# Kernel tuning notes

Hardware: AMD Instinct MI355X
Metric: run time of the kernel (lower is better)

Reference implementation:

```python
import jax, jax.numpy as jnp
import numpy as np

GAMMA = 1.0
ALPHA = 0.5
EPS = 1e-8


def setup_inputs() -> dict:
    key = jax.random.key(0)
    k1, k2 = jax.random.split(key)
    x = jax.random.normal(k1, (2048, 32), dtype=jnp.float32)
    y = jax.random.normal(k2, (2048, 32), dtype=jnp.float32)
    return {"x": x, "y": y}


def _normalize(a):
    # torch: mean/std over batch dim, std is unbiased (ddof=1)
    mu = jnp.mean(a, axis=0, keepdims=True)
    sd = jnp.std(a, axis=0, ddof=1, keepdims=True)
    return (a - mu) / (sd + EPS)


def reference(x, y):
    # Classical RBF kernel on normalized inputs
    xn = _normalize(x)
    yn = _normalize(y)
    d = xn[:, None, :] - yn[None, :, :]            # [N, M, D]
    classical = jnp.exp(-GAMMA * jnp.sum(d * d, axis=-1))  # [N, M]

    # Quantum kernel, analytic closed form:
    # RY(t)|0> = [cos(t/2), sin(t/2)]; product state overlap ->
    # |<psi_x|psi_y>|^2 = prod_i cos^2((x_i - y_i)/2)
    qd = (x[:, None, :] - y[None, :, :]) * 0.5     # [N, M, D]
    quantum = jnp.prod(jnp.square(jnp.cos(qd)), axis=-1)    # [N, M]

    return (1.0 - ALPHA) * classical + ALPHA * quantum
```

## Files before the change

### kernel.cpp

```cpp
#include <hip/hip_runtime.h>
#include <math.h>

#define NROWS 2048
#define DDIM 32

typedef __attribute__((ext_vector_type(8))) short short8;
typedef __attribute__((ext_vector_type(4))) float f32x4;
typedef __attribute__((ext_vector_type(2))) float f32x2;

__device__ __forceinline__ unsigned packbf(float a, float b) {
  return (__float_as_uint(a) >> 16) | (__float_as_uint(b) & 0xffff0000u);
}

__global__ __launch_bounds__(512, 2) void HybridKernel_fused(
    const float* __restrict__ x, const float* __restrict__ y,
    float* __restrict__ out) {
  __shared__ f32x4 sCSx[16 * 128];
  __shared__ f32x4 sYP[2048];
  __shared__ uint4 sXB[2][2][128 * 5];
  __shared__ f32x4 sRed[2][64][8];
  __shared__ f32x4 sRedQ[2][64][8];
  __shared__ float sNrm[2][128];
  __shared__ float sMu[2][32];
  __shared__ float sInv[2][32];

  const int t = threadIdx.x;
  const int i0 = blockIdx.y * 128;
  const int j0 = blockIdx.x * 128;

  float4 gx[2], gy[2];
#pragma unroll
  for (int rep = 0; rep < 2; ++rep) {
    const int u = t + 512 * rep;
    const int row = u >> 3;
    const int q = u & 7;
    gx[rep] = *reinterpret_cast<const float4*>(&x[(i0 + row) * DDIM + q * 4]);
    gy[rep] = *reinterpret_cast<const float4*>(&y[(j0 + row) * DDIM + q * 4]);
  }

#pragma unroll
  for (int rep = 0; rep < 2; ++rep) {
    const int u = t + 512 * rep;
    const int row = u >> 3;
    const int q = u & 7;
    {
      const float4 g = gx[rep];
      const float gv[4] = {g.x, g.y, g.z, g.w};
      float hc[4], hs[4];
#pragma unroll
      for (int k = 0; k < 4; ++k) {
        float sn, cs;
        __sincosf(gv[k], &sn, &cs);
        hc[k] = 0.5f * cs;
        hs[k] = 0.5f * sn;
      }
      const int dp0 = 2 * q, dp1 = 2 * q + 1;
      sCSx[dp0 * 128 + (row ^ (dp0 & 7))] = f32x4{hc[0], hs[0], hc[1], hs[1]};
      sCSx[dp1 * 128 + (row ^ (dp1 & 7))] = f32x4{hc[2], hs[2], hc[3], hs[3]};
    }
    {
      const float4 g = gy[rep];
      const float gv[4] = {g.x, g.y, g.z, g.w};
      float hc[4], hs[4];
#pragma unroll
      for (int k = 0; k < 4; ++k) {
        float sn, cs;
        __sincosf(gv[k], &sn, &cs);
        hc[k] = cs;
        hs[k] = sn;
      }
      const int gblk = row >> 5;
      const int h = (row >> 4) & 1;
      const int p = row & 15;
#pragma unroll
      for (int e = 0; e < 2; ++e) {
        const int dp = 2 * q + e;
        const int pp = p ^ dp;
        float* bA = (float*)&sYP[(dp * 8 + 2 * gblk + 0) * 16 + pp];
        float* bB = (float*)&sYP[(dp * 8 + 2 * gblk + 1) * 16 + pp];
        bA[h] = hc[2 * e];
        bA[2 + h] = hs[2 * e];
        bB[h] = hc[2 * e + 1];
        bB[2 + h] = hs[2 * e + 1];
      }
    }
  }

  {
    const int cq = t & 7;
    const int rg = t >> 3;
    const f32x4* px = reinterpret_cast<const f32x4*>(x) + rg * 8 + cq;
    const f32x4* py = reinterpret_cast<const f32x4*>(y) + rg * 8 + cq;
    f32x4 sx = {0.f, 0.f, 0.f, 0.f}, qx = {0.f, 0.f, 0.f, 0.f};
    f32x4 sy = {0.f, 0.f, 0.f, 0.f}, qy = {0.f, 0.f, 0.f, 0.f};
#pragma unroll 4
    for (int i = 0; i < NROWS / 64; ++i) {
      const f32x4 vx = px[(size_t)i * 64 * 8];
      const f32x4 vy = py[(size_t)i * 64 * 8];
      sx += vx;
      qx = __builtin_elementwise_fma(vx, vx, qx);
      sy += vy;
      qy = __builtin_elementwise_fma(vy, vy, qy);
    }
    sRed[0][rg][cq] = sx;
    sRedQ[0][rg][cq] = qx;
    sRed[1][rg][cq] = sy;
    sRedQ[1][rg][cq] = qy;
  }
  __syncthreads();
  if (t < 128) {
    const int a = t >> 6;
    const int g8 = (t >> 3) & 7;
    const int cq2 = t & 7;
    f32x4 S = {0.f, 0.f, 0.f, 0.f}, Q = {0.f, 0.f, 0.f, 0.f};
#pragma unroll
    for (int k = 0; k < 8; ++k) {
      S += sRed[a][g8 * 8 + k][cq2];
      Q += sRedQ[a][g8 * 8 + k][cq2];
    }
    sRed[a][g8][cq2] = S;
    sRedQ[a][g8][cq2] = Q;
  }
  __syncthreads();
  if (t < 16) {
    const int a = t >> 3;
    const int cq2 = t & 7;
    f32x4 S = {0.f, 0.f, 0.f, 0.f}, Q = {0.f, 0.f, 0.f, 0.f};
#pragma unroll
    for (int k = 0; k < 8; ++k) {
      S += sRed[a][k][cq2];
      Q += sRedQ[a][k][cq2];
    }
    const float n = (float)NROWS;
#pragma unroll
    for (int k = 0; k < 4; ++k) {
      const float mean = S[k] / n;
      const float var = fmaxf((Q[k] - S[k] * mean) / (n - 1.f), 0.f);
      sMu[a][cq2 * 4 + k] = mean;
      sInv[a][cq2 * 4 + k] = 1.f / (sqrtf(var) + 1e-8f);
    }
  }
  __syncthreads();

#pragma unroll
  for (int rep = 0; rep < 2; ++rep) {
    const int u = t + 512 * rep;
    const int row = u >> 3;
    const int q = u & 7;
#pragma unroll
    for (int side = 0; side < 2; ++side) {
      const float4 g = side ? gy[rep] : gx[rep];
      const float gv[4] = {g.x, g.y, g.z, g.w};
      float xn[4];
      float nrm = 0.f;
#pragma unroll
      for (int k = 0; k < 4; ++k) {
        const int d = q * 4 + k;
        xn[k] = (gv[k] - sMu[side][d]) * sInv[side][d];
        nrm = fmaf(xn[k], xn[k], nrm);
      }
      float hif[4], lof[4];
#pragma unroll
      for (int k = 0; k < 4; ++k) {
        hif[k] = __uint_as_float(__float_as_uint(xn[k]) & 0xffff0000u);
        lof[k] = xn[k] - hif[k];
      }
      char* bh = (char*)&sXB[side][0][0] + row * 80 + q * 8;
      char* bl = (char*)&sXB[side][1][0] + row * 80 + q * 8;
      *reinterpret_cast<uint2*>(bh) =
          make_uint2(packbf(hif[0], hif[1]), packbf(hif[2], hif[3]));
      *reinterpret_cast<uint2*>(bl) =
          make_uint2(packbf(lof[0], lof[1]), packbf(lof[2], lof[3]));
      nrm += __shfl_xor(nrm, 1);
      nrm += __shfl_xor(nrm, 2);
      nrm += __shfl_xor(nrm, 4);
      if ((t & 7) == 0) sNrm[side][row] = nrm;
    }
  }
  __syncthreads();

  const int w = t >> 6;
  const int l = t & 63;
  const int l4 = l >> 4;
  const int ln = l & 15;
  const int R0 = (w >> 1) * 32;
  const int C0 = (w & 1) * 64;

  int r_idx[8], c_idx[4];
#pragma unroll
  for (int ri = 0; ri < 8; ++ri)
    r_idx[ri] = R0 + 16 * (ri >> 2) + 4 * l4 + (ri & 3);
#pragma unroll
  for (int tc = 0; tc < 4; ++tc) c_idx[tc] = C0 + 16 * tc + ln;

  short8 Ah[2], Al[2], Bh[4], Bl[4];
  {
    const char* bxh = (const char*)&sXB[0][0][0];
    const char* bxl = (const char*)&sXB[0][1][0];
    const char* byh = (const char*)&sXB[1][0][0];
    const char* byl = (const char*)&sXB[1][1][0];
#pragma unroll
    for (int tr = 0; tr < 2; ++tr) {
      const int off = (R0 + 16 * tr + ln) * 80 + l4 * 16;
      Ah[tr] = *reinterpret_cast<const short8*>(bxh + off);
      Al[tr] = *reinterpret_cast<const short8*>(bxl + off);
    }
#pragma unroll
    for (int tc = 0; tc < 4; ++tc) {
      const int off = (C0 + 16 * tc + ln) * 80 + l4 * 16;
      Bh[tc] = *reinterpret_cast<const short8*>(byh + off);
      Bl[tc] = *reinterpret_cast<const short8*>(byl + off);
    }
  }
  f32x4 dotacc[2][4];
#pragma unroll
  for (int tr = 0; tr < 2; ++tr)
#pragma unroll
    for (int tc = 0; tc < 4; ++tc) {
      f32x4 a = {0.f, 0.f, 0.f, 0.f};
      a = __builtin_amdgcn_mfma_f32_16x16x32_bf16(Ah[tr], Bl[tc], a, 0, 0, 0);
      a = __builtin_amdgcn_mfma_f32_16x16x32_bf16(Al[tr], Bh[tc], a, 0, 0, 0);
      a = __builtin_amdgcn_mfma_f32_16x16x32_bf16(Ah[tr], Bh[tc], a, 0, 0, 0);
      dotacc[tr][tc] = a;
    }

  const int gBase = C0 >> 5;
  f32x2 qp01[8], qp23[8];
#pragma unroll
  for (int ri = 0; ri < 8; ++ri) {
    qp01[ri] = f32x2{1.f, 1.f};
    qp23[ri] = f32x2{1.f, 1.f};
  }

#pragma unroll
  for (int dp = 0; dp < 16; ++dp) {
    const int swx = dp & 7;
    const int pp = ln ^ dp;
    const f32x4 A0 = sYP[(dp * 8 + 2 * gBase + 0) * 16 + pp];
    const f32x4 B0 = sYP[(dp * 8 + 2 * gBase + 1) * 16 + pp];
    const f32x4 A1 = sYP[(dp * 8 + 2 * (gBase + 1) + 0) * 16 + pp];
    const f32x4 B1 = sYP[(dp * 8 + 2 * (gBase + 1) + 1) * 16 + pp];
    const f32x2 h2 = {0.5f, 0.5f};
#pragma unroll
    for (int ri = 0; ri < 8; ++ri) {
      const f32x4 fx = sCSx[dp * 128 + (r_idx[ri] ^ swx)];
      f32x2 i0 = __builtin_elementwise_fma(fx.yy, A0.zw, h2);
      f32x2 t0 = __builtin_elementwise_fma(fx.xx, A0.xy, i0);
      f32x2 i1 = __builtin_elementwise_fma(fx.ww, B0.zw, h2);
      f32x2 t1 = __builtin_elementwise_fma(fx.zz, B0.xy, i1);
      qp01[ri] *= t0 * t1;
      f32x2 i2 = __builtin_elementwise_fma(fx.yy, A1.zw, h2);
      f32x2 t2 = __builtin_elementwise_fma(fx.xx, A1.xy, i2);
      f32x2 i3 = __builtin_elementwise_fma(fx.ww, B1.zw, h2);
      f32x2 t3 = __builtin_elementwise_fma(fx.zz, B1.xy, i3);
      qp23[ri] *= t2 * t3;
    }
  }

#pragma unroll
  for (int tr = 0; tr < 2; ++tr) {
#pragma unroll
    for (int mm = 0; mm < 4; ++mm) {
      const int ri = tr * 4 + mm;
      const float nx = sNrm[0][r_idx[ri]];
      float* o = out + (size_t)(i0 + r_idx[ri]) * NROWS + j0;
#pragma unroll
      for (int tc = 0; tc < 4; ++tc) {
        const float ny = sNrm[1][c_idx[tc]];
        const float cl = __expf(2.f * dotacc[tr][tc][mm] - nx - ny);
        const float qv = (tc < 2) ? qp01[ri][tc] : qp23[ri][tc - 2];
        o[c_idx[tc]] = 0.5f * (cl + qv);
      }
    }
  }
}

extern "C" void kernel_launch(void* const* d_in, const int* in_sizes, int n_in,
                              void* d_out, int out_size, void* d_ws,
                              size_t ws_size, hipStream_t stream) {
  const float* x = (const float*)d_in[0];
  const float* y = (const float*)d_in[1];
  float* out = (float*)d_out;

  dim3 grid(NROWS / 128, NROWS / 128);
  HybridKernel_fused<<<grid, 512, 0, stream>>>(x, y, out);
}
```

Baseline: 24.78 us.

## Store quantum-kernel cos/sin tables as packed fp16 in a unified LDS layout

```diff
diff --git a/kernel.cpp b/kernel.cpp
--- a/kernel.cpp
+++ b/kernel.cpp
@@ -1,4 +1,5 @@
 #include <hip/hip_runtime.h>
+#include <hip/hip_fp16.h>
 #include <math.h>
 
 #define NROWS 2048
@@ -6,7 +7,11 @@
 
 typedef __attribute__((ext_vector_type(8))) short short8;
 typedef __attribute__((ext_vector_type(4))) float f32x4;
-typedef __attribute__((ext_vector_type(2))) float f32x2;
+
+union H8 {
+  _Float16 h[8];
+  uint4 u;
+};
 
 __device__ __forceinline__ unsigned packbf(float a, float b) {
   return (__float_as_uint(a) >> 16) | (__float_as_uint(b) & 0xffff0000u);
@@ -15,8 +20,7 @@
 __global__ __launch_bounds__(512, 2) void HybridKernel_fused(
     const float* __restrict__ x, const float* __restrict__ y,
     float* __restrict__ out) {
-  __shared__ f32x4 sCSx[16 * 128];
-  __shared__ f32x4 sYP[2048];
+  __shared__ uint4 sCSh[2][8 * 128];
   __shared__ uint4 sXB[2][2][128 * 5];
   __shared__ f32x4 sRed[2][64][8];
   __shared__ f32x4 sRedQ[2][64][8];
@@ -43,46 +47,20 @@
     const int u = t + 512 * rep;
     const int row = u >> 3;
     const int q = u & 7;
-    {
-      const float4 g = gx[rep];
+#pragma unroll
+    for (int side = 0; side < 2; ++side) {
+      const float4 g = side ? gy[rep] : gx[rep];
+      const float sc = side ? 1.0f : 0.5f;
       const float gv[4] = {g.x, g.y, g.z, g.w};
-      float hc[4], hs[4];
+      H8 pk;
 #pragma unroll
       for (int k = 0; k < 4; ++k) {
         float sn, cs;
         __sincosf(gv[k], &sn, &cs);
-        hc[k] = 0.5f * cs;
-        hs[k] = 0.5f * sn;
-      }
-      const int dp0 = 2 * q, dp1 = 2 * q + 1;
-      sCSx[dp0 * 128 + (row ^ (dp0 & 7))] = f32x4{hc[0], hs[0], hc[1], hs[1]};
-      sCSx[dp1 * 128 + (row ^ (dp1 & 7))] = f32x4{hc[2], hs[2], hc[3], hs[3]};
-    }
-    {
-      const float4 g = gy[rep];
-      const float gv[4] = {g.x, g.y, g.z, g.w};
-      float hc[4], hs[4];
-#pragma unroll
-      for (int k = 0; k < 4; ++k) {
-        float sn, cs;
-        __sincosf(gv[k], &sn, &cs);
-        hc[k] = cs;
-        hs[k] = sn;
-      }
-      const int gblk = row >> 5;
-      const int h = (row >> 4) & 1;
-      const int p = row & 15;
-#pragma unroll
-      for (int e = 0; e < 2; ++e) {
-        const int dp = 2 * q + e;
-        const int pp = p ^ dp;
-        float* bA = (float*)&sYP[(dp * 8 + 2 * gblk + 0) * 16 + pp];
-        float* bB = (float*)&sYP[(dp * 8 + 2 * gblk + 1) * 16 + pp];
-        bA[h] = hc[2 * e];
-        bA[2 + h] = hs[2 * e];
-        bB[h] = hc[2 * e + 1];
-        bB[2 + h] = hs[2 * e + 1];
-      }
+        pk.h[2 * k] = (_Float16)(sc * cs);
+        pk.h[2 * k + 1] = (_Float16)(sc * sn);
+      }
+      sCSh[side][q * 128 + (row ^ q)] = pk.u;
     }
   }
 
@@ -224,36 +202,36 @@
       dotacc[tr][tc] = a;
     }
 
-  const int gBase = C0 >> 5;
-  f32x2 qp01[8], qp23[8];
-#pragma unroll
-  for (int ri = 0; ri < 8; ++ri) {
-    qp01[ri] = f32x2{1.f, 1.f};
-    qp23[ri] = f32x2{1.f, 1.f};
-  }
-
-#pragma unroll
-  for (int dp = 0; dp < 16; ++dp) {
-    const int swx = dp & 7;
-    const int pp = ln ^ dp;
-    const f32x4 A0 = sYP[(dp * 8 + 2 * gBase + 0) * 16 + pp];
-    const f32x4 B0 = sYP[(dp * 8 + 2 * gBase + 1) * 16 + pp];
-    const f32x4 A1 = sYP[(dp * 8 + 2 * (gBase + 1) + 0) * 16 + pp];
-    const f32x4 B1 = sYP[(dp * 8 + 2 * (gBase + 1) + 1) * 16 + pp];
-    const f32x2 h2 = {0.5f, 0.5f};
+  const uint4* sCS0 = &sCSh[0][0];
+  const uint4* sCS1 = &sCSh[1][0];
+  float qp[8][4];
+#pragma unroll
+  for (int ri = 0; ri < 8; ++ri)
+#pragma unroll
+    for (int tc = 0; tc < 4; ++tc) qp[ri][tc] = 1.f;
+
+#pragma unroll
+  for (int q = 0; q < 8; ++q) {
+    const int base = q * 128;
+    H8 fy[4];
+#pragma unroll
+    for (int tc = 0; tc < 4; ++tc) fy[tc].u = sCS1[base + (c_idx[tc] ^ q)];
 #pragma unroll
     for (int ri = 0; ri < 8; ++ri) {
-      const f32x4 fx = sCSx[dp * 128 + (r_idx[ri] ^ swx)];
-      f32x2 i0 = __builtin_elementwise_fma(fx.yy, A0.zw, h2);
-      f32x2 t0 = __builtin_elementwise_fma(fx.xx, A0.xy, i0);
-      f32x2 i1 = __builtin_elementwise_fma(fx.ww, B0.zw, h2);
-      f32x2 t1 = __builtin_elementwise_fma(fx.zz, B0.xy, i1);
-      qp01[ri] *= t0 * t1;
-      f32x2 i2 = __builtin_elementwise_fma(fx.yy, A1.zw, h2);
-      f32x2 t2 = __builtin_elementwise_fma(fx.xx, A1.xy, i2);
-      f32x2 i3 = __builtin_elementwise_fma(fx.ww, B1.zw, h2);
-      f32x2 t3 = __builtin_elementwise_fma(fx.zz, B1.xy, i3);
-      qp23[ri] *= t2 * t3;
+      H8 fx;
+      fx.u = sCS0[base + (r_idx[ri] ^ q)];
+#pragma unroll
+      for (int tc = 0; tc < 4; ++tc) {
+        const float t0 = fmaf((float)fx.h[0], (float)fy[tc].h[0],
+                              fmaf((float)fx.h[1], (float)fy[tc].h[1], 0.5f));
+        const float t1 = fmaf((float)fx.h[2], (float)fy[tc].h[2],
+                              fmaf((float)fx.h[3], (float)fy[tc].h[3], 0.5f));
+        const float t2 = fmaf((float)fx.h[4], (float)fy[tc].h[4],
+                              fmaf((float)fx.h[5], (float)fy[tc].h[5], 0.5f));
+        const float t3 = fmaf((float)fx.h[6], (float)fy[tc].h[6],
+                              fmaf((float)fx.h[7], (float)fy[tc].h[7], 0.5f));
+        qp[ri][tc] *= (t0 * t1) * (t2 * t3);
+      }
     }
   }
 
@@ -268,8 +246,7 @@
       for (int tc = 0; tc < 4; ++tc) {
         const float ny = sNrm[1][c_idx[tc]];
         const float cl = __expf(2.f * dotacc[tr][tc][mm] - nx - ny);
-        const float qv = (tc < 2) ? qp01[ri][tc] : qp23[ri][tc - 2];
-        o[c_idx[tc]] = 0.5f * (cl + qv);
+        o[c_idx[tc]] = 0.5f * (cl + qp[ri][tc]);
       }
     }
   }
```

New measurement: 27.78 us. 12.1% more time.
